# Optimization experiments

Measured on AMD Instinct MI355X. Metric: run time of the kernel, lower is better.

## Reference

```python
import jax, jax.numpy as jnp
import numpy as np

B, S, E, H = 2, 2048, 512, 8
MLP = 4 * E


def _ln(x, w, b, eps=1e-5):
    m = jnp.mean(x, -1, keepdims=True)
    v = jnp.var(x, -1, keepdims=True)
    return (x - m) / jnp.sqrt(v + eps) * w + b


def setup_inputs() -> dict:
    key = jax.random.key(0)
    ks = jax.random.split(key, 8)
    s = lambda k, shape: (jax.random.normal(k, shape, jnp.float32) * 0.02)
    return {
        "query": jax.random.normal(ks[0], (B, S, E), jnp.float32),
        "attn_gate": jax.random.uniform(ks[1], (B * H, S, S), jnp.float32),
        "in_proj_w": s(ks[2], (3 * E, E)),
        "in_proj_b": jnp.zeros((3 * E,), jnp.float32),
        "out_w": s(ks[3], (E, E)),
        "out_b": jnp.zeros((E,), jnp.float32),
        "ln1_w": jnp.ones((E,), jnp.float32),
        "ln1_b": jnp.zeros((E,), jnp.float32),
        "ln2_w": jnp.ones((E,), jnp.float32),
        "ln2_b": jnp.zeros((E,), jnp.float32),
        "w1": s(ks[4], (MLP, E)),
        "b1": jnp.zeros((MLP,), jnp.float32),
        "w2": s(ks[5], (E, MLP)),
        "b2": jnp.zeros((E,), jnp.float32),
    }


def reference(query, attn_gate, in_proj_w, in_proj_b, out_w, out_b,
              ln1_w, ln1_b, ln2_w, ln2_b, w1, b1, w2, b2):
    b, s, e = query.shape
    h = H
    dh = e // h
    nq = _ln(query, ln1_w, ln1_b)  # pre-LN; key=value=normed query (self-attn)
    Wq, Wk, Wv = jnp.split(in_proj_w, 3, axis=0)
    bq, bk, bv = jnp.split(in_proj_b, 3, axis=0)
    q = nq @ Wq.T + bq
    k = nq @ Wk.T + bk
    v = nq @ Wv.T + bv
    # faithful raw reshape (B,S,E)->(B*H,S,Dh), as in the torch .view
    q = q.reshape(b * h, s, dh)
    k = k.reshape(b * h, s, dh)
    v = v.reshape(b * h, s, dh)
    w = jnp.einsum("bqd,bkd->bqk", q, k)  # no 1/sqrt(d) scaling in source
    w = w * attn_gate
    w = w / (jnp.sum(w, -1, keepdims=True) + 1e-12)  # sum-renormalization
    w = jax.nn.softmax(w, axis=-1)
    o = jnp.einsum("bqk,bkd->bqd", w, v)  # (B*H, S, Dh)
    o = jnp.swapaxes(o, 0, 1).reshape(s, b, e)  # faithful transpose+view
    o = o @ out_w.T + out_b
    o = jnp.swapaxes(o, 0, 1)  # back to batch_first (B,S,E)
    x = query + o
    hmid = _ln(x, ln2_w, ln2_b)
    x = x + (jax.nn.gelu(hmid @ w1.T + b1, approximate=False) @ w2.T + b2)
    attn_weights = w.reshape(b, h, s, s).mean(axis=1)  # average_attn_weights=True
    return (x, attn_weights)
```

## Files before the change

kernel.cpp:

```cpp
#include <hip/hip_runtime.h>
#include <cstdint>
#include <cstddef>

typedef __bf16 bf16_t;
typedef __bf16 bf16x8 __attribute__((ext_vector_type(8)));
typedef float  f32x4  __attribute__((ext_vector_type(4)));

#define S_LEN   2048
#define E_DIM   512
#define H_NUM   8
#define DH      64
#define MLP_DIM 2048

static __device__ __forceinline__ unsigned short f2bfu(float f){
  bf16_t h = (bf16_t)f;
  return __builtin_bit_cast(unsigned short, h);
}

static __device__ __forceinline__ float gelu_f(float v){
  return 0.5f*v*(1.0f + erff(v*0.70710678118654752f));
}

__global__ __launch_bounds__(256) void cvt_kernel(const float* __restrict__ s,
                                                  bf16_t* __restrict__ d, int n){
  int i = (blockIdx.x*256 + threadIdx.x)*4;
  if (i < n){
    float4 v = *(const float4*)(s + i);
    ushort4 pk;
    pk.x = f2bfu(v.x); pk.y = f2bfu(v.y); pk.z = f2bfu(v.z); pk.w = f2bfu(v.w);
    *(ushort4*)((unsigned short*)d + i) = pk;
  }
}

__global__ __launch_bounds__(256) void cvt_split_kernel(const float* __restrict__ s,
                                                        bf16_t* __restrict__ dh,
                                                        bf16_t* __restrict__ dl, int n){
  int i = (blockIdx.x*256 + threadIdx.x)*4;
  if (i < n){
    float4 v = *(const float4*)(s + i);
    float xs[4] = {v.x, v.y, v.z, v.w};
    ushort4 ph, pl;
    unsigned short* hp = (unsigned short*)&ph;
    unsigned short* lp = (unsigned short*)&pl;
    #pragma unroll
    for (int j=0;j<4;j++){
      bf16_t hi = (bf16_t)xs[j];
      bf16_t lo = (bf16_t)(xs[j] - (float)hi);
      hp[j] = __builtin_bit_cast(unsigned short, hi);
      lp[j] = __builtin_bit_cast(unsigned short, lo);
    }
    *(ushort4*)((unsigned short*)dh + i) = ph;
    *(ushort4*)((unsigned short*)dl + i) = pl;
  }
}

__global__ __launch_bounds__(256) void ln_kernel(const float* __restrict__ x,
                                                 const float* __restrict__ w,
                                                 const float* __restrict__ bb,
                                                 bf16_t* __restrict__ out){
  const int row  = blockIdx.x*4 + (threadIdx.x>>6);
  const int lane = threadIdx.x & 63;
  const float* xr = x + (size_t)row*E_DIM + lane*8;
  float4 v0 = *(const float4*)xr;
  float4 v1 = *(const float4*)(xr + 4);
  float xs[8] = {v0.x, v0.y, v0.z, v0.w, v1.x, v1.y, v1.z, v1.w};
  float s = 0.f, s2 = 0.f;
  #pragma unroll
  for (int j=0;j<8;j++){ s += xs[j]; s2 += xs[j]*xs[j]; }
  #pragma unroll
  for (int off=1; off<64; off<<=1){
    s  += __shfl_xor(s,  off, 64);
    s2 += __shfl_xor(s2, off, 64);
  }
  float mean = s*(1.f/512.f);
  float var  = s2*(1.f/512.f) - mean*mean;
  float rstd = rsqrtf(fmaxf(var, 0.f) + 1e-5f);
  const float* wp = w  + lane*8;
  const float* bp = bb + lane*8;
  bf16x8 ov;
  #pragma unroll
  for (int j=0;j<8;j++)
    ov[j] = (bf16_t)((xs[j]-mean)*rstd*wp[j] + bp[j]);
  *(bf16x8*)(out + (size_t)row*E_DIM + lane*8) = ov;
}

__global__ __launch_bounds__(256) void ln_split_kernel(const float* __restrict__ x,
                                                       const float* __restrict__ w,
                                                       const float* __restrict__ bb,
                                                       bf16_t* __restrict__ oh,
                                                       bf16_t* __restrict__ ol){
  const int row  = blockIdx.x*4 + (threadIdx.x>>6);
  const int lane = threadIdx.x & 63;
  const float* xr = x + (size_t)row*E_DIM + lane*8;
  float4 v0 = *(const float4*)xr;
  float4 v1 = *(const float4*)(xr + 4);
  float xs[8] = {v0.x, v0.y, v0.z, v0.w, v1.x, v1.y, v1.z, v1.w};
  float s = 0.f, s2 = 0.f;
  #pragma unroll
  for (int j=0;j<8;j++){ s += xs[j]; s2 += xs[j]*xs[j]; }
  #pragma unroll
  for (int off=1; off<64; off<<=1){
    s  += __shfl_xor(s,  off, 64);
    s2 += __shfl_xor(s2, off, 64);
  }
  float mean = s*(1.f/512.f);
  float var  = s2*(1.f/512.f) - mean*mean;
  float rstd = rsqrtf(fmaxf(var, 0.f) + 1e-5f);
  const float* wp = w  + lane*8;
  const float* bp = bb + lane*8;
  bf16x8 vh, vl;
  #pragma unroll
  for (int j=0;j<8;j++){
    float v = (xs[j]-mean)*rstd*wp[j] + bp[j];
    bf16_t hi = (bf16_t)v;
    vh[j] = hi;
    vl[j] = (bf16_t)(v - (float)hi);
  }
  size_t o = (size_t)row*E_DIM + lane*8;
  *(bf16x8*)(oh + o) = vh;
  *(bf16x8*)(ol + o) = vl;
}

__global__ __launch_bounds__(256) void gemm_qkv_split(
    const bf16_t* __restrict__ Ah, const bf16_t* __restrict__ Al,
    const bf16_t* __restrict__ Bh, const bf16_t* __restrict__ Bl,
    const float* __restrict__ bias,
    bf16_t* __restrict__ qh, bf16_t* __restrict__ ql,
    bf16_t* __restrict__ kh, bf16_t* __restrict__ kl,
    bf16_t* __restrict__ vtmp)
{
  constexpr int TM = 128, TN = 64, BK = 64, MI = 4, NI = 2;
  const int K = 512;

  __shared__ bf16_t Ahs[TM*BK], Als[TM*BK];
  __shared__ bf16_t Bhs[TN*BK], Bls[TN*BK];

  const int tid  = threadIdx.x;
  const int wave = tid>>6, lane = tid&63, quad = lane>>4, l16 = lane&15;
  const int wm = wave>>1, wn = wave&1;

  const int nblk = 1536/TN;
  const int bm = blockIdx.x / nblk;
  const int bn = blockIdx.x % nblk;
  const int m0 = bm*TM, n0 = bn*TN;

  f32x4 acc[MI][NI];
  #pragma unroll
  for (int i=0;i<MI;i++)
    #pragma unroll
    for (int j=0;j<NI;j++)
      acc[i][j] = (f32x4){0.f,0.f,0.f,0.f};

  for (int k0 = 0; k0 < K; k0 += BK){
    bf16x8 avh[4], avl[4], bvh[2], bvl[2];
    #pragma unroll
    for (int i=0;i<4;i++){
      int ga = tid + i*256;
      int row = ga>>3, c8 = (ga&7) ^ (row&7);
      size_t off = (size_t)(m0+row)*K + k0 + c8*8;
      avh[i] = *(const bf16x8*)(Ah + off);
      avl[i] = *(const bf16x8*)(Al + off);
    }
    #pragma unroll
    for (int i=0;i<2;i++){
      int gb = tid + i*256;
      int row = gb>>3, c8 = (gb&7) ^ (row&7);
      size_t off = (size_t)(n0+row)*K + k0 + c8*8;
      bvh[i] = *(const bf16x8*)(Bh + off);
      bvl[i] = *(const bf16x8*)(Bl + off);
    }
    __syncthreads();
    #pragma unroll
    for (int i=0;i<4;i++){
      *(bf16x8*)(Ahs + (size_t)(tid + i*256)*8) = avh[i];
      *(bf16x8*)(Als + (size_t)(tid + i*256)*8) = avl[i];
    }
    #pragma unroll
    for (int i=0;i<2;i++){
      *(bf16x8*)(Bhs + (size_t)(tid + i*256)*8) = bvh[i];
      *(bf16x8*)(Bls + (size_t)(tid + i*256)*8) = bvl[i];
    }
    __syncthreads();
    #pragma unroll
    for (int ks=0;ks<2;ks++){
      bf16x8 afh[MI], afl[MI], bfh[NI], bfl[NI];
      #pragma unroll
      for (int mi=0;mi<MI;mi++){
        int rm = wm*64 + mi*16 + l16;
        size_t sl = (size_t)(rm*8 + ((ks*4+quad) ^ (rm&7)))*8;
        afh[mi] = *(const bf16x8*)(Ahs + sl);
        afl[mi] = *(const bf16x8*)(Als + sl);
      }
      #pragma unroll
      for (int ni=0;ni<NI;ni++){
        int rn = wn*32 + ni*16 + l16;
        size_t sl = (size_t)(rn*8 + ((ks*4+quad) ^ (rn&7)))*8;
        bfh[ni] = *(const bf16x8*)(Bhs + sl);
        bfl[ni] = *(const bf16x8*)(Bls + sl);
      }
      #pragma unroll
      for (int mi=0;mi<MI;mi++)
        #pragma unroll
        for (int ni=0;ni<NI;ni++){
          acc[mi][ni] = __builtin_amdgcn_mfma_f32_16x16x32_bf16(afh[mi], bfh[ni], acc[mi][ni], 0,0,0);
          acc[mi][ni] = __builtin_amdgcn_mfma_f32_16x16x32_bf16(afl[mi], bfh[ni], acc[mi][ni], 0,0,0);
          acc[mi][ni] = __builtin_amdgcn_mfma_f32_16x16x32_bf16(afh[mi], bfl[ni], acc[mi][ni], 0,0,0);
        }
    }
  }

  #pragma unroll
  for (int mi=0;mi<MI;mi++){
    const int grow0 = m0 + wm*64 + mi*16 + quad*4;
    #pragma unroll
    for (int ni=0;ni<NI;ni++){
      const int gcol = n0 + wn*32 + ni*16 + l16;
      const float bvx = bias[gcol];
      if (gcol < 512){
        #pragma unroll
        for (int r=0;r<4;r++){
          float v = acc[mi][ni][r] + bvx;
          size_t idx = (size_t)(grow0+r)*E_DIM + gcol;
          bf16_t hi = (bf16_t)v;
          qh[idx] = hi;
          ql[idx] = (bf16_t)(v - (float)hi);
        }
      } else if (gcol < 1024){
        const int cc = gcol - 512;
        #pragma unroll
        for (int r=0;r<4;r++){
          float v = acc[mi][ni][r] + bvx;
          size_t idx = (size_t)(grow0+r)*E_DIM + cc;
          bf16_t hi = (bf16_t)v;
          kh[idx] = hi;
          kl[idx] = (bf16_t)(v - (float)hi);
        }
      } else {
        const int cc = gcol - 1024;
        #pragma unroll
        for (int r=0;r<4;r++)
          vtmp[(size_t)(grow0+r)*E_DIM + cc] = (bf16_t)(acc[mi][ni][r] + bvx);
      }
    }
  }
}

__global__ __launch_bounds__(256) void vtrans_kernel(const bf16_t* __restrict__ v,
                                                     bf16_t* __restrict__ vt){
  __shared__ bf16_t tile[32*516];
  const int ic = blockIdx.x >> 3;
  const int rg = blockIdx.x & 7;
  const int tid = threadIdx.x;
  const size_t src = ((size_t)ic*256 + rg*32)*E_DIM;
  #pragma unroll
  for (int j=0;j<8;j++){
    int idx = j*2048 + tid*8;
    int row = idx >> 9, col = idx & 511;
    *(bf16x8*)(tile + row*516 + col) = *(const bf16x8*)(v + src + idx);
  }
  __syncthreads();
  #pragma unroll
  for (int j=0;j<8;j++){
    int idx = j*2048 + tid*8;
    int d = idx >> 8;
    int toff = idx & 255;
    int row = toff >> 3;
    bf16x8 o;
    #pragma unroll
    for (int jj=0;jj<8;jj++)
      o[jj] = tile[row*516 + jj*64 + d];
    *(bf16x8*)(vt + ((size_t)ic*64 + d)*S_LEN + rg*256 + toff) = o;
  }
}

template<int TN, int MODE>
__global__ __launch_bounds__(256) void gemm_kernel(
    const bf16_t* __restrict__ A, const bf16_t* __restrict__ Bw,
    const float* __restrict__ bias, int M, int N, int K,
    void* out0, const float* __restrict__ resid)
{
  constexpr int TM = 128;
  constexpr int BK = 64;
  constexpr int MI = 4;
  constexpr int NI = TN/32;
  constexpr int GB = TN/32;

  __shared__ bf16_t As[TM*BK];
  __shared__ bf16_t Bs[TN*BK];

  const int tid  = threadIdx.x;
  const int wave = tid>>6, lane = tid&63, quad = lane>>4, l16 = lane&15;
  const int wm = wave>>1, wn = wave&1;

  const int nblk = N / TN;
  const int bm = blockIdx.x / nblk;
  const int bn = blockIdx.x % nblk;
  const int m0 = bm*TM, n0 = bn*TN;

  f32x4 acc[MI][NI];
  #pragma unroll
  for (int i=0;i<MI;i++)
    #pragma unroll
    for (int j=0;j<NI;j++)
      acc[i][j] = (f32x4){0.f,0.f,0.f,0.f};

  for (int k0 = 0; k0 < K; k0 += BK){
    bf16x8 av[4];
    #pragma unroll
    for (int i=0;i<4;i++){
      int ga = tid + i*256;
      int row = ga>>3, c8 = (ga&7) ^ (row&7);
      av[i] = *(const bf16x8*)(A + (size_t)(m0+row)*K + k0 + c8*8);
    }
    bf16x8 bv[GB];
    #pragma unroll
    for (int i=0;i<GB;i++){
      int gb = tid + i*256;
      int row = gb>>3, c8 = (gb&7) ^ (row&7);
      bv[i] = *(const bf16x8*)(Bw + (size_t)(n0+row)*K + k0 + c8*8);
    }
    __syncthreads();
    #pragma unroll
    for (int i=0;i<4;i++)  *(bf16x8*)(As + (size_t)(tid + i*256)*8) = av[i];
    #pragma unroll
    for (int i=0;i<GB;i++) *(bf16x8*)(Bs + (size_t)(tid + i*256)*8) = bv[i];
    __syncthreads();
    #pragma unroll
    for (int ks=0;ks<2;ks++){
      bf16x8 af[MI], bfr[NI];
      #pragma unroll
      for (int mi=0;mi<MI;mi++){
        int rm = wm*64 + mi*16 + l16;
        af[mi] = *(const bf16x8*)(As + (size_t)(rm*8 + ((ks*4+quad) ^ (rm&7)))*8);
      }
      #pragma unroll
      for (int ni=0;ni<NI;ni++){
        int rn = wn*(TN/2) + ni*16 + l16;
        bfr[ni] = *(const bf16x8*)(Bs + (size_t)(rn*8 + ((ks*4+quad) ^ (rn&7)))*8);
      }
      #pragma unroll
      for (int mi=0;mi<MI;mi++)
        #pragma unroll
        for (int ni=0;ni<NI;ni++)
          acc[mi][ni] = __builtin_amdgcn_mfma_f32_16x16x32_bf16(af[mi], bfr[ni], acc[mi][ni], 0,0,0);
    }
  }

  #pragma unroll
  for (int mi=0;mi<MI;mi++){
    const int grow0 = m0 + wm*64 + mi*16 + quad*4;
    #pragma unroll
    for (int ni=0;ni<NI;ni++){
      const int gcol = n0 + wn*(TN/2) + ni*16 + l16;
      const float bvx = bias[gcol];
      if constexpr (MODE==1){
        float* xo = (float*)out0;
        #pragma unroll
        for (int r=0;r<4;r++){
          size_t idx = (size_t)(grow0+r)*E_DIM + gcol;
          xo[idx] = resid[idx] + acc[mi][ni][r] + bvx;
        }
      } else if constexpr (MODE==2){
        bf16_t* hp = (bf16_t*)out0;
        #pragma unroll
        for (int r=0;r<4;r++)
          hp[(size_t)(grow0+r)*MLP_DIM + gcol] = (bf16_t)gelu_f(acc[mi][ni][r] + bvx);
      } else {
        float* xo = (float*)out0;
        #pragma unroll
        for (int r=0;r<4;r++){
          size_t idx = (size_t)(grow0+r)*E_DIM + gcol;
          xo[idx] = xo[idx] + acc[mi][ni][r] + bvx;
        }
      }
    }
  }
}

__global__ __launch_bounds__(1024) void attn_kernel(
    const bf16_t* __restrict__ qhb, const bf16_t* __restrict__ qlb,
    const bf16_t* __restrict__ khb, const bf16_t* __restrict__ klb,
    const bf16_t* __restrict__ vt,  const float* __restrict__ gate,
    bf16_t* __restrict__ og, float* __restrict__ aw)
{
  __shared__ float  u_s[16*2052];
  __shared__ double red_d[16*16];
  __shared__ float  red_m[2*16*16];
  __shared__ float  osh[16*64];
  __shared__ float  zsh[16];
  __shared__ float  invr_sh[16];
  __shared__ float  msh[16];

  const int bid = blockIdx.x;
  const int c = bid & 7;
  const int t = bid >> 3;
  const int h = t & 7;
  const int g = t >> 3;
  const int gi = g*8 + c;
  const int b  = gi >> 7;
  const int sqt = gi & 127;
  const int bh = b*H_NUM + h;
  const int sq0 = sqt*16;

  const int tid = threadIdx.x;
  const int wave = tid>>6, lane = tid&63, quad = lane>>4, l16 = lane&15;

  if (tid < 16*64) osh[tid] = 0.f;
  if (tid >= 1008) zsh[tid-1008] = 0.f;

  bf16x8 qah0, qah1, qal0, qal1;
  {
    const size_t qoff = ((size_t)bh*S_LEN + sq0 + l16)*DH + quad*8;
    qah0 = *(const bf16x8*)(qhb + qoff);
    qah1 = *(const bf16x8*)(qhb + qoff + 32);
    qal0 = *(const bf16x8*)(qlb + qoff);
    qal1 = *(const bf16x8*)(qlb + qoff + 32);
  }

  double sums[4] = {0.0,0.0,0.0,0.0};
  float maxs[4], mins[4];
  #pragma unroll
  for (int r=0;r<4;r++){ maxs[r] = -__builtin_inff(); mins[r] = __builtin_inff(); }

  const size_t gate_row = ((size_t)bh*S_LEN + sq0 + quad*4)*S_LEN;

  for (int cb = wave; cb < 32; cb += 16){
    #pragma unroll
    for (int nb=0; nb<4; nb++){
      const int col0 = cb*64 + nb*16;
      const size_t koff = ((size_t)bh*S_LEN + col0 + l16)*DH + quad*8;
      bf16x8 khf0 = *(const bf16x8*)(khb + koff);
      bf16x8 khf1 = *(const bf16x8*)(khb + koff + 32);
      bf16x8 klf0 = *(const bf16x8*)(klb + koff);
      bf16x8 klf1 = *(const bf16x8*)(klb + koff + 32);
      const int sk = col0 + l16;
      const float* gp = gate + gate_row + sk;
      float gv[4];
      #pragma unroll
      for (int r=0;r<4;r++) gv[r] = gp[(size_t)r*S_LEN];
      f32x4 acc = (f32x4){0.f,0.f,0.f,0.f};
      acc = __builtin_amdgcn_mfma_f32_16x16x32_bf16(qah0, khf0, acc, 0,0,0);
      acc = __builtin_amdgcn_mfma_f32_16x16x32_bf16(qah1, khf1, acc, 0,0,0);
      acc = __builtin_amdgcn_mfma_f32_16x16x32_bf16(qal0, khf0, acc, 0,0,0);
      acc = __builtin_amdgcn_mfma_f32_16x16x32_bf16(qal1, khf1, acc, 0,0,0);
      acc = __builtin_amdgcn_mfma_f32_16x16x32_bf16(qah0, klf0, acc, 0,0,0);
      acc = __builtin_amdgcn_mfma_f32_16x16x32_bf16(qah1, klf1, acc, 0,0,0);
      #pragma unroll
      for (int r=0;r<4;r++){
        float u = acc[r]*gv[r];
        u_s[(quad*4+r)*2052 + sk] = u;
        sums[r] += (double)u;
        maxs[r] = fmaxf(maxs[r], u);
        mins[r] = fminf(mins[r], u);
      }
    }
  }

  #pragma unroll
  for (int off=1; off<16; off<<=1){
    #pragma unroll
    for (int r=0;r<4;r++){
      sums[r] += __shfl_xor(sums[r], off, 64);
      maxs[r] = fmaxf(maxs[r], __shfl_xor(maxs[r], off, 64));
      mins[r] = fminf(mins[r], __shfl_xor(mins[r], off, 64));
    }
  }
  if (l16 == 0){
    #pragma unroll
    for (int r=0;r<4;r++){
      red_d[wave*16 + quad*4 + r] = sums[r];
      red_m[(0*16 + wave)*16 + quad*4 + r] = maxs[r];
      red_m[(1*16 + wave)*16 + quad*4 + r] = mins[r];
    }
  }
  __syncthreads();
  if (tid < 16){
    double sm = 0.0;
    float mx = -__builtin_inff(), mn = __builtin_inff();
    #pragma unroll
    for (int w=0; w<16; w++){
      sm += red_d[w*16 + tid];
      mx = fmaxf(mx, red_m[(0*16 + w)*16 + tid]);
      mn = fminf(mn, red_m[(1*16 + w)*16 + tid]);
    }
    double rsum = sm + 1e-12;
    float inv = (float)(1.0/rsum);
    invr_sh[tid] = inv;
    msh[tid] = (rsum > 0.0 ? mx : mn) * inv;
  }
  __syncthreads();

  const float inv_r = invr_sh[l16];
  const float m_v   = msh[l16];
  const int nb2 = wave & 3, kh2 = wave >> 2;
  f32x4 oacc = (f32x4){0.f,0.f,0.f,0.f};
  float zp = 0.f;
  const bf16_t* vbase = vt + ((size_t)bh*DH + nb2*16 + l16)*S_LEN;
  const float* urow = &u_s[l16*2052];
  for (int kc = kh2*16; kc < kh2*16 + 16; kc++){
    const int k0 = kc*32 + quad*8;
    float4 u0 = *(const float4*)(urow + k0);
    float4 u1 = *(const float4*)(urow + k0 + 4);
    float e0 = __expf(u0.x*inv_r - m_v);
    float e1 = __expf(u0.y*inv_r - m_v);
    float e2 = __expf(u0.z*inv_r - m_v);
    float e3 = __expf(u0.w*inv_r - m_v);
    float e4 = __expf(u1.x*inv_r - m_v);
    float e5 = __expf(u1.y*inv_r - m_v);
    float e6 = __expf(u1.z*inv_r - m_v);
    float e7 = __expf(u1.w*inv_r - m_v);
    if (nb2 == 0) zp += ((e0+e1)+(e2+e3)) + ((e4+e5)+(e6+e7));
    bf16x8 pa;
    pa[0]=(bf16_t)e0; pa[1]=(bf16_t)e1; pa[2]=(bf16_t)e2; pa[3]=(bf16_t)e3;
    pa[4]=(bf16_t)e4; pa[5]=(bf16_t)e5; pa[6]=(bf16_t)e6; pa[7]=(bf16_t)e7;
    bf16x8 vf = *(const bf16x8*)(vbase + k0);
    oacc = __builtin_amdgcn_mfma_f32_16x16x32_bf16(pa, vf, oacc, 0,0,0);
  }
  if (nb2 == 0){
    zp += __shfl_xor(zp, 16, 64);
    zp += __shfl_xor(zp, 32, 64);
    if (lane < 16) atomicAdd(&zsh[l16], zp);
  }
  #pragma unroll
  for (int r=0;r<4;r++)
    atomicAdd(&osh[(quad*4+r)*64 + nb2*16 + l16], oacc[r]);
  __syncthreads();

  const int bq = bh >> 3, hh = bh & 7;
  if (tid < 16*64){
    int r = tid >> 6, d = tid & 63;
    float val = osh[tid] / zsh[r];
    og[((size_t)(bq*S_LEN + sq0 + r))*E_DIM + hh*DH + d] = (bf16_t)val;
  }

  const int r3 = tid >> 6;
  const float inv3 = invr_sh[r3], m3 = msh[r3];
  const float sc = 0.125f / zsh[r3];
  float* awrow = aw + ((size_t)(bq*S_LEN) + sq0 + r3)*S_LEN;
  const float* ur3 = &u_s[r3*2052];
  for (int col = lane; col < S_LEN; col += 64){
    float e = __expf(ur3[col]*inv3 - m3);
    atomicAdd(&awrow[col], e*sc);
  }
}

extern "C" void kernel_launch(void* const* d_in, const int* in_sizes, int n_in,
                              void* d_out, int out_size, void* d_ws, size_t ws_size,
                              hipStream_t stream)
{
  const float* query     = (const float*)d_in[0];
  const float* gate      = (const float*)d_in[1];
  const float* in_proj_w = (const float*)d_in[2];
  const float* in_proj_b = (const float*)d_in[3];
  const float* out_w     = (const float*)d_in[4];
  const float* out_b     = (const float*)d_in[5];
  const float* ln1_w     = (const float*)d_in[6];
  const float* ln1_b     = (const float*)d_in[7];
  const float* ln2_w     = (const float*)d_in[8];
  const float* ln2_b     = (const float*)d_in[9];
  const float* w1        = (const float*)d_in[10];
  const float* b1        = (const float*)d_in[11];
  const float* w2        = (const float*)d_in[12];
  const float* b2        = (const float*)d_in[13];

  char* ws = (char*)d_ws;
  bf16_t* nqh   = (bf16_t*)(ws);
  bf16_t* nql   = (bf16_t*)(ws + ((size_t)4<<20));
  bf16_t* qh    = (bf16_t*)(ws + ((size_t)8<<20));
  bf16_t* ql    = (bf16_t*)(ws + ((size_t)12<<20));
  bf16_t* kh    = (bf16_t*)(ws + ((size_t)16<<20));
  bf16_t* kl    = (bf16_t*)(ws + ((size_t)20<<20));
  bf16_t* vtmp  = (bf16_t*)(ws + ((size_t)24<<20));
  bf16_t* vt    = (bf16_t*)(ws + ((size_t)28<<20));
  bf16_t* og    = (bf16_t*)(ws + ((size_t)32<<20));
  bf16_t* hmid  = (bf16_t*)(ws + ((size_t)36<<20));
  bf16_t* h1    = (bf16_t*)(ws + ((size_t)40<<20));
  bf16_t* wqh   = (bf16_t*)(ws + ((size_t)56<<20));
  bf16_t* wql   = (bf16_t*)(ws + ((size_t)58<<20));
  bf16_t* woutb = (bf16_t*)(ws + ((size_t)60<<20));
  bf16_t* w1b   = (bf16_t*)(ws + ((size_t)61<<20));
  bf16_t* w2b   = (bf16_t*)(ws + ((size_t)63<<20));

  float* xout = (float*)d_out;
  float* aw   = xout + (size_t)2*S_LEN*E_DIM;

  hipMemsetAsync(aw, 0, (size_t)2*S_LEN*S_LEN*sizeof(float), stream);

  cvt_split_kernel<<<768, 256, 0, stream>>>(in_proj_w, wqh, wql, 786432);
  cvt_kernel<<<256, 256, 0, stream>>>(out_w, woutb, 262144);
  cvt_kernel<<<1024,256, 0, stream>>>(w1,    w1b,   1048576);
  cvt_kernel<<<1024,256, 0, stream>>>(w2,    w2b,   1048576);

  ln_split_kernel<<<1024, 256, 0, stream>>>(query, ln1_w, ln1_b, nqh, nql);

  gemm_qkv_split<<<768, 256, 0, stream>>>(nqh, nql, wqh, wql, in_proj_b,
                                          qh, ql, kh, kl, vtmp);

  vtrans_kernel<<<128, 256, 0, stream>>>(vtmp, vt);

  attn_kernel<<<2048, 1024, 0, stream>>>(qh, ql, kh, kl, vt, gate, og, aw);

  gemm_kernel<64,1><<<256, 256, 0, stream>>>(og, woutb, out_b,
      4096, 512, 512, (void*)xout, query);

  ln_kernel<<<1024, 256, 0, stream>>>(xout, ln2_w, ln2_b, hmid);

  gemm_kernel<128,2><<<512, 256, 0, stream>>>(hmid, w1b, b1,
      4096, 2048, 512, (void*)h1, nullptr);

  gemm_kernel<64,3><<<256, 256, 0, stream>>>(h1, w2b, b2,
      4096, 512, 2048, (void*)xout, nullptr);
}
```

Before: 825.6 us.

## Loop heads inside attention block and accumulate averaged weights in registers

Each attention block now handles one 16-query tile for all 8 heads in sequence, not one head per block. The head-averaged attention weights build up in registers and are written once with nontemporal stores. This removes the global atomicAdds and the memset of the attention-weights buffer, and gate loads become nontemporal. The cost is 256 blocks instead of 2048 with a serial head loop, so parallelism drops and there may be too few blocks to fill the GPU.

```diff
diff --git a/kernel.cpp b/kernel.cpp
--- a/kernel.cpp
+++ b/kernel.cpp
@@ -391,157 +391,165 @@
   __shared__ float  invr_sh[16];
   __shared__ float  msh[16];
 
-  const int bid = blockIdx.x;
-  const int c = bid & 7;
-  const int t = bid >> 3;
-  const int h = t & 7;
-  const int g = t >> 3;
-  const int gi = g*8 + c;
-  const int b  = gi >> 7;
-  const int sqt = gi & 127;
-  const int bh = b*H_NUM + h;
+  const int b   = blockIdx.x >> 7;
+  const int sqt = blockIdx.x & 127;
   const int sq0 = sqt*16;
 
   const int tid = threadIdx.x;
   const int wave = tid>>6, lane = tid&63, quad = lane>>4, l16 = lane&15;
-
-  if (tid < 16*64) osh[tid] = 0.f;
-  if (tid >= 1008) zsh[tid-1008] = 0.f;
-
-  bf16x8 qah0, qah1, qal0, qal1;
-  {
-    const size_t qoff = ((size_t)bh*S_LEN + sq0 + l16)*DH + quad*8;
-    qah0 = *(const bf16x8*)(qhb + qoff);
-    qah1 = *(const bf16x8*)(qhb + qoff + 32);
-    qal0 = *(const bf16x8*)(qlb + qoff);
-    qal1 = *(const bf16x8*)(qlb + qoff + 32);
-  }
-
-  double sums[4] = {0.0,0.0,0.0,0.0};
-  float maxs[4], mins[4];
-  #pragma unroll
-  for (int r=0;r<4;r++){ maxs[r] = -__builtin_inff(); mins[r] = __builtin_inff(); }
-
-  const size_t gate_row = ((size_t)bh*S_LEN + sq0 + quad*4)*S_LEN;
-
-  for (int cb = wave; cb < 32; cb += 16){
-    #pragma unroll
-    for (int nb=0; nb<4; nb++){
-      const int col0 = cb*64 + nb*16;
-      const size_t koff = ((size_t)bh*S_LEN + col0 + l16)*DH + quad*8;
-      bf16x8 khf0 = *(const bf16x8*)(khb + koff);
-      bf16x8 khf1 = *(const bf16x8*)(khb + koff + 32);
-      bf16x8 klf0 = *(const bf16x8*)(klb + koff);
-      bf16x8 klf1 = *(const bf16x8*)(klb + koff + 32);
-      const int sk = col0 + l16;
-      const float* gp = gate + gate_row + sk;
-      float gv[4];
-      #pragma unroll
-      for (int r=0;r<4;r++) gv[r] = gp[(size_t)r*S_LEN];
-      f32x4 acc = (f32x4){0.f,0.f,0.f,0.f};
-      acc = __builtin_amdgcn_mfma_f32_16x16x32_bf16(qah0, khf0, acc, 0,0,0);
-      acc = __builtin_amdgcn_mfma_f32_16x16x32_bf16(qah1, khf1, acc, 0,0,0);
-      acc = __builtin_amdgcn_mfma_f32_16x16x32_bf16(qal0, khf0, acc, 0,0,0);
-      acc = __builtin_amdgcn_mfma_f32_16x16x32_bf16(qal1, khf1, acc, 0,0,0);
-      acc = __builtin_amdgcn_mfma_f32_16x16x32_bf16(qah0, klf0, acc, 0,0,0);
-      acc = __builtin_amdgcn_mfma_f32_16x16x32_bf16(qah1, klf1, acc, 0,0,0);
+  const int row16 = tid >> 6;
+
+  float awacc[32];
+  #pragma unroll
+  for (int j=0;j<32;j++) awacc[j] = 0.f;
+
+  for (int h = 0; h < H_NUM; h++){
+    const int bh = b*H_NUM + h;
+
+    osh[tid & 1023] = 0.f;
+    if (tid < 16) zsh[tid] = 0.f;
+
+    bf16x8 qah0, qah1, qal0, qal1;
+    {
+      const size_t qoff = ((size_t)bh*S_LEN + sq0 + l16)*DH + quad*8;
+      qah0 = *(const bf16x8*)(qhb + qoff);
+      qah1 = *(const bf16x8*)(qhb + qoff + 32);
+      qal0 = *(const bf16x8*)(qlb + qoff);
+      qal1 = *(const bf16x8*)(qlb + qoff + 32);
+    }
+
+    double sums[4] = {0.0,0.0,0.0,0.0};
+    float maxs[4], mins[4];
+    #pragma unroll
+    for (int r=0;r<4;r++){ maxs[r] = -__builtin_inff(); mins[r] = __builtin_inff(); }
+
+    const size_t gate_row = ((size_t)bh*S_LEN + sq0 + quad*4)*S_LEN;
+
+    for (int cb = wave; cb < 32; cb += 16){
+      #pragma unroll
+      for (int nb=0; nb<4; nb++){
+        const int col0 = cb*64 + nb*16;
+        const size_t koff = ((size_t)bh*S_LEN + col0 + l16)*DH + quad*8;
+        bf16x8 khf0 = *(const bf16x8*)(khb + koff);
+        bf16x8 khf1 = *(const bf16x8*)(khb + koff + 32);
+        bf16x8 klf0 = *(const bf16x8*)(klb + koff);
+        bf16x8 klf1 = *(const bf16x8*)(klb + koff + 32);
+        const int sk = col0 + l16;
+        const float* gp = gate + gate_row + sk;
+        float gv[4];
+        #pragma unroll
+        for (int r=0;r<4;r++) gv[r] = __builtin_nontemporal_load(gp + (size_t)r*S_LEN);
+        f32x4 acc = (f32x4){0.f,0.f,0.f,0.f};
+        acc = __builtin_amdgcn_mfma_f32_16x16x32_bf16(qah0, khf0, acc, 0,0,0);
+        acc = __builtin_amdgcn_mfma_f32_16x16x32_bf16(qah1, khf1, acc, 0,0,0);
+        acc = __builtin_amdgcn_mfma_f32_16x16x32_bf16(qal0, khf0, acc, 0,0,0);
+        acc = __builtin_amdgcn_mfma_f32_16x16x32_bf16(qal1, khf1, acc, 0,0,0);
+        acc = __builtin_amdgcn_mfma_f32_16x16x32_bf16(qah0, klf0, acc, 0,0,0);
+        acc = __builtin_amdgcn_mfma_f32_16x16x32_bf16(qah1, klf1, acc, 0,0,0);
+        #pragma unroll
+        for (int r=0;r<4;r++){
+          float u = acc[r]*gv[r];
+          u_s[(quad*4+r)*2052 + sk] = u;
+          sums[r] += (double)u;
+          maxs[r] = fmaxf(maxs[r], u);
+          mins[r] = fminf(mins[r], u);
+        }
+      }
+    }
+
+    #pragma unroll
+    for (int off=1; off<16; off<<=1){
       #pragma unroll
       for (int r=0;r<4;r++){
-        float u = acc[r]*gv[r];
-        u_s[(quad*4+r)*2052 + sk] = u;
-        sums[r] += (double)u;
-        maxs[r] = fmaxf(maxs[r], u);
-        mins[r] = fminf(mins[r], u);
-      }
-    }
-  }
-
-  #pragma unroll
-  for (int off=1; off<16; off<<=1){
-    #pragma unroll
-    for (int r=0;r<4;r++){
-      sums[r] += __shfl_xor(sums[r], off, 64);
-      maxs[r] = fmaxf(maxs[r], __shfl_xor(maxs[r], off, 64));
-      mins[r] = fminf(mins[r], __shfl_xor(mins[r], off, 64));
-    }
-  }
-  if (l16 == 0){
-    #pragma unroll
-    for (int r=0;r<4;r++){
-      red_d[wave*16 + quad*4 + r] = sums[r];
-      red_m[(0*16 + wave)*16 + quad*4 + r] = maxs[r];
-      red_m[(1*16 + wave)*16 + quad*4 + r] = mins[r];
-    }
-  }
-  __syncthreads();
-  if (tid < 16){
-    double sm = 0.0;
-    float mx = -__builtin_inff(), mn = __builtin_inff();
-    #pragma unroll
-    for (int w=0; w<16; w++){
-      sm += red_d[w*16 + tid];
-      mx = fmaxf(mx, red_m[(0*16 + w)*16 + tid]);
-      mn = fminf(mn, red_m[(1*16 + w)*16 + tid]);
-    }
-    double rsum = sm + 1e-12;
-    float inv = (float)(1.0/rsum);
-    invr_sh[tid] = inv;
-    msh[tid] = (rsum > 0.0 ? mx : mn) * inv;
-  }
-  __syncthreads();
-
-  const float inv_r = invr_sh[l16];
-  const float m_v   = msh[l16];
-  const int nb2 = wave & 3, kh2 = wave >> 2;
-  f32x4 oacc = (f32x4){0.f,0.f,0.f,0.f};
-  float zp = 0.f;
-  const bf16_t* vbase = vt + ((size_t)bh*DH + nb2*16 + l16)*S_LEN;
-  const float* urow = &u_s[l16*2052];
-  for (int kc = kh2*16; kc < kh2*16 + 16; kc++){
-    const int k0 = kc*32 + quad*8;
-    float4 u0 = *(const float4*)(urow + k0);
-    float4 u1 = *(const float4*)(urow + k0 + 4);
-    float e0 = __expf(u0.x*inv_r - m_v);
-    float e1 = __expf(u0.y*inv_r - m_v);
-    float e2 = __expf(u0.z*inv_r - m_v);
-    float e3 = __expf(u0.w*inv_r - m_v);
-    float e4 = __expf(u1.x*inv_r - m_v);
-    float e5 = __expf(u1.y*inv_r - m_v);
-    float e6 = __expf(u1.z*inv_r - m_v);
-    float e7 = __expf(u1.w*inv_r - m_v);
-    if (nb2 == 0) zp += ((e0+e1)+(e2+e3)) + ((e4+e5)+(e6+e7));
-    bf16x8 pa;
-    pa[0]=(bf16_t)e0; pa[1]=(bf16_t)e1; pa[2]=(bf16_t)e2; pa[3]=(bf16_t)e3;
-    pa[4]=(bf16_t)e4; pa[5]=(bf16_t)e5; pa[6]=(bf16_t)e6; pa[7]=(bf16_t)e7;
-    bf16x8 vf = *(const bf16x8*)(vbase + k0);
-    oacc = __builtin_amdgcn_mfma_f32_16x16x32_bf16(pa, vf, oacc, 0,0,0);
-  }
-  if (nb2 == 0){
-    zp += __shfl_xor(zp, 16, 64);
-    zp += __shfl_xor(zp, 32, 64);
-    if (lane < 16) atomicAdd(&zsh[l16], zp);
-  }
-  #pragma unroll
-  for (int r=0;r<4;r++)
-    atomicAdd(&osh[(quad*4+r)*64 + nb2*16 + l16], oacc[r]);
-  __syncthreads();
-
-  const int bq = bh >> 3, hh = bh & 7;
-  if (tid < 16*64){
-    int r = tid >> 6, d = tid & 63;
-    float val = osh[tid] / zsh[r];
-    og[((size_t)(bq*S_LEN + sq0 + r))*E_DIM + hh*DH + d] = (bf16_t)val;
-  }
-
-  const int r3 = tid >> 6;
-  const float inv3 = invr_sh[r3], m3 = msh[r3];
-  const float sc = 0.125f / zsh[r3];
-  float* awrow = aw + ((size_t)(bq*S_LEN) + sq0 + r3)*S_LEN;
-  const float* ur3 = &u_s[r3*2052];
-  for (int col = lane; col < S_LEN; col += 64){
-    float e = __expf(ur3[col]*inv3 - m3);
-    atomicAdd(&awrow[col], e*sc);
-  }
+        sums[r] += __shfl_xor(sums[r], off, 64);
+        maxs[r] = fmaxf(maxs[r], __shfl_xor(maxs[r], off, 64));
+        mins[r] = fminf(mins[r], __shfl_xor(mins[r], off, 64));
+      }
+    }
+    if (l16 == 0){
+      #pragma unroll
+      for (int r=0;r<4;r++){
+        red_d[wave*16 + quad*4 + r] = sums[r];
+        red_m[(0*16 + wave)*16 + quad*4 + r] = maxs[r];
+        red_m[(1*16 + wave)*16 + quad*4 + r] = mins[r];
+      }
+    }
+    __syncthreads();
+    if (tid < 16){
+      double sm = 0.0;
+      float mx = -__builtin_inff(), mn = __builtin_inff();
+      #pragma unroll
+      for (int w=0; w<16; w++){
+        sm += red_d[w*16 + tid];
+        mx = fmaxf(mx, red_m[(0*16 + w)*16 + tid]);
+        mn = fminf(mn, red_m[(1*16 + w)*16 + tid]);
+      }
+      double rsum = sm + 1e-12;
+      float inv = (float)(1.0/rsum);
+      invr_sh[tid] = inv;
+      msh[tid] = (rsum > 0.0 ? mx : mn) * inv;
+    }
+    __syncthreads();
+
+    const float inv_r = invr_sh[l16];
+    const float m_v   = msh[l16];
+    const int nb2 = wave & 3, kh2 = wave >> 2;
+    f32x4 oacc = (f32x4){0.f,0.f,0.f,0.f};
+    float zp = 0.f;
+    const bf16_t* vbase = vt + ((size_t)bh*DH + nb2*16 + l16)*S_LEN;
+    const float* urow = &u_s[l16*2052];
+    for (int kc = kh2*16; kc < kh2*16 + 16; kc++){
+      const int k0 = kc*32 + quad*8;
+      float4 u0 = *(const float4*)(urow + k0);
+      float4 u1 = *(const float4*)(urow + k0 + 4);
+      float e0 = __expf(u0.x*inv_r - m_v);
+      float e1 = __expf(u0.y*inv_r - m_v);
+      float e2 = __expf(u0.z*inv_r - m_v);
+      float e3 = __expf(u0.w*inv_r - m_v);
+      float e4 = __expf(u1.x*inv_r - m_v);
+      float e5 = __expf(u1.y*inv_r - m_v);
+      float e6 = __expf(u1.z*inv_r - m_v);
+      float e7 = __expf(u1.w*inv_r - m_v);
+      if (nb2 == 0) zp += ((e0+e1)+(e2+e3)) + ((e4+e5)+(e6+e7));
+      bf16x8 pa;
+      pa[0]=(bf16_t)e0; pa[1]=(bf16_t)e1; pa[2]=(bf16_t)e2; pa[3]=(bf16_t)e3;
+      pa[4]=(bf16_t)e4; pa[5]=(bf16_t)e5; pa[6]=(bf16_t)e6; pa[7]=(bf16_t)e7;
+      bf16x8 vf = *(const bf16x8*)(vbase + k0);
+      oacc = __builtin_amdgcn_mfma_f32_16x16x32_bf16(pa, vf, oacc, 0,0,0);
+    }
+    if (nb2 == 0){
+      zp += __shfl_xor(zp, 16, 64);
+      zp += __shfl_xor(zp, 32, 64);
+      if (lane < 16) atomicAdd(&zsh[l16], zp);
+    }
+    #pragma unroll
+    for (int r=0;r<4;r++)
+      atomicAdd(&osh[(quad*4+r)*64 + nb2*16 + l16], oacc[r]);
+    __syncthreads();
+
+    {
+      int r = tid >> 6, d = tid & 63;
+      float val = osh[tid] / zsh[r];
+      og[((size_t)(b*S_LEN + sq0 + r))*E_DIM + h*DH + d] = (bf16_t)val;
+    }
+
+    {
+      const float inv3 = invr_sh[row16], m3 = msh[row16];
+      const float sc = 0.125f / zsh[row16];
+      const float* ur = &u_s[row16*2052];
+      #pragma unroll
+      for (int j=0;j<32;j++){
+        float e = __expf(ur[j*64 + lane]*inv3 - m3);
+        awacc[j] = fmaf(e, sc, awacc[j]);
+      }
+    }
+    __syncthreads();
+  }
+
+  float* awrow = aw + ((size_t)(b*S_LEN) + sq0 + row16)*S_LEN;
+  #pragma unroll
+  for (int j=0;j<32;j++)
+    __builtin_nontemporal_store(awacc[j], awrow + j*64 + lane);
 }
 
 extern "C" void kernel_launch(void* const* d_in, const int* in_sizes, int n_in,
@@ -584,8 +592,6 @@
   float* xout = (float*)d_out;
   float* aw   = xout + (size_t)2*S_LEN*E_DIM;
 
-  hipMemsetAsync(aw, 0, (size_t)2*S_LEN*S_LEN*sizeof(float), stream);
-
   cvt_split_kernel<<<768, 256, 0, stream>>>(in_proj_w, wqh, wql, 786432);
   cvt_kernel<<<256, 256, 0, stream>>>(out_w, woutb, 262144);
   cvt_kernel<<<1024,256, 0, stream>>>(w1,    w1b,   1048576);
@@ -598,7 +604,7 @@
 
   vtrans_kernel<<<128, 256, 0, stream>>>(vtmp, vt);
 
-  attn_kernel<<<2048, 1024, 0, stream>>>(qh, ql, kh, kl, vt, gate, og, aw);
+  attn_kernel<<<256, 1024, 0, stream>>>(qh, ql, kh, kl, vt, gate, og, aw);
 
   gemm_kernel<64,1><<<256, 256, 0, stream>>>(og, woutb, out_b,
       4096, 512, 512, (void*)xout, query);
```

New measurement: 746.6 us. 1.11x faster.
